# Kernel tuning notes

Measured on AMD Instinct MI355X. Metric: run time of the kernel, lower is better.

## Reference

```python
import jax, jax.numpy as jnp
import numpy as np

OUTPUT_SEQ_LEN = 64


def setup_inputs() -> dict:
    key = jax.random.key(0)
    ks = jax.random.split(key, 12)
    S, B, H, O = 256, 256, 512, 64  # src_len, batch, hidden, output vocab
    sos_token = jax.random.normal(ks[0], (1, B, O), dtype=jnp.float32)
    h = jax.random.normal(ks[1], (1, B, H), dtype=jnp.float32)
    encoder_outputs = jax.random.normal(ks[2], (S, B, H), dtype=jnp.float32)
    s = 0.05
    params = {
        'Wa': jax.random.normal(ks[3], (2 * H, H), dtype=jnp.float32) * s,  # attn linear
        'ba': jnp.zeros((H,), dtype=jnp.float32),
        'v': jax.random.normal(ks[4], (H,), dtype=jnp.float32) * s,          # scoring vector
        'W_ih': jax.random.normal(ks[5], (H, O + H), dtype=jnp.float32) * s,
        'b_ih': jnp.zeros((H,), dtype=jnp.float32),
        'W_hh': jax.random.normal(ks[6], (H, H), dtype=jnp.float32) * s,
        'b_hh': jnp.zeros((H,), dtype=jnp.float32),
        'Wo': jax.random.normal(ks[7], (O, H), dtype=jnp.float32) * s,       # output linear
        'bo': jnp.zeros((O,), dtype=jnp.float32),
    }
    return {'sos_token': sos_token, 'h': h, 'encoder_outputs': encoder_outputs, **params}


def reference(sos_token, h, encoder_outputs, Wa, ba, v, W_ih, b_ih, W_hh, b_hh, Wo, bo):
    # predict=True path of Decoder.forward: greedy argmax feedback each step.
    O = sos_token.shape[-1]
    h0 = h[0]                      # [B, H]
    x0 = sos_token[0]              # [B, O]

    def step(carry, _):
        h_t, x_t = carry           # [B,H], [B,O]
        # Bahdanau attention: score over source positions (softmax over dim 0)
        hid = jnp.broadcast_to(h_t[None], encoder_outputs.shape)          # [S,B,H]
        energy = jnp.tanh(jnp.concatenate([hid, encoder_outputs], axis=2) @ Wa + ba)  # [S,B,H]
        score = energy @ v                                                # [S,B]
        attn = jax.nn.softmax(score, axis=0)                              # [S,B]
        context = jnp.einsum('sb,sbh->bh', attn, encoder_outputs)         # [B,H]
        # single-layer vanilla RNN cell
        rnn_in = jnp.concatenate([x_t, context], axis=1)                  # [B,O+H]
        h_new = jnp.tanh(rnn_in @ W_ih.T + b_ih + h_t @ W_hh.T + b_hh)    # [B,H]
        out = h_new @ Wo.T + bo                                           # [B,O]
        # greedy feedback: one_hot(argmax(softmax(out))) == one_hot(argmax(out))
        x_next = jax.nn.one_hot(jnp.argmax(out, axis=1), O, dtype=out.dtype)
        return (h_new, x_next), out

    _, outs = jax.lax.scan(step, (h0, x0), None, length=OUTPUT_SEQ_LEN)   # [T,B,O]
    preds = outs[: OUTPUT_SEQ_LEN - 1]                                    # [T-1,B,O]
    preds = jnp.transpose(preds, (1, 2, 0))                               # [B,O,T-1]
    return preds
```

## Files before the change

kernel.cpp:

```cpp
#include <hip/hip_runtime.h>
#include <math.h>

#define SS 256
#define BB 256
#define HH 512
#define OO 64
#define NSTEP 63

__global__ __launch_bounds__(256) void k_ew_gemm(const float* __restrict__ A,
                                                 const float* __restrict__ Bm,
                                                 float* __restrict__ C)
{
    __shared__ float As[8][132];
    __shared__ float Bs[8][132];
    const int tid = threadIdx.x;
    const int bm = blockIdx.x * 128;
    const int bn = blockIdx.y * 128;
    const int tx = tid & 15;
    const int ty = tid >> 4;
    const int a_row = tid >> 1;
    const int a_k4 = (tid & 1) * 4;
    const int b_row = tid >> 5;
    const int b_n4 = (tid & 31) * 4;

    float acc[8][8];
#pragma unroll
    for (int i = 0; i < 8; i++)
#pragma unroll
        for (int j = 0; j < 8; j++) acc[i][j] = 0.f;

    for (int kt = 0; kt < 512; kt += 8) {
        float4 av = *(const float4*)(A + (size_t)(bm + a_row) * 512 + kt + a_k4);
        As[a_k4 + 0][a_row] = av.x;
        As[a_k4 + 1][a_row] = av.y;
        As[a_k4 + 2][a_row] = av.z;
        As[a_k4 + 3][a_row] = av.w;
        *(float4*)(&Bs[b_row][b_n4]) = *(const float4*)(Bm + (size_t)(kt + b_row) * 512 + bn + b_n4);
        __syncthreads();
#pragma unroll
        for (int kk = 0; kk < 8; kk++) {
            float av8[8], bv8[8];
            *(float4*)&av8[0] = *(const float4*)&As[kk][ty * 4];
            *(float4*)&av8[4] = *(const float4*)&As[kk][64 + ty * 4];
            *(float4*)&bv8[0] = *(const float4*)&Bs[kk][tx * 4];
            *(float4*)&bv8[4] = *(const float4*)&Bs[kk][64 + tx * 4];
#pragma unroll
            for (int i = 0; i < 8; i++)
#pragma unroll
                for (int j = 0; j < 8; j++) acc[i][j] += av8[i] * bv8[j];
        }
        __syncthreads();
    }
#pragma unroll
    for (int i = 0; i < 8; i++) {
        int m = bm + ((i < 4) ? (ty * 4 + i) : (64 + ty * 4 + i - 4));
        int mrow = (m & 255) * 256 + (m >> 8);
        float4 o0 = make_float4(acc[i][0], acc[i][1], acc[i][2], acc[i][3]);
        float4 o1 = make_float4(acc[i][4], acc[i][5], acc[i][6], acc[i][7]);
        *(float4*)(C + (size_t)mrow * 512 + bn + tx * 4) = o0;
        *(float4*)(C + (size_t)mrow * 512 + bn + 64 + tx * 4) = o1;
    }
}

__global__ __launch_bounds__(256) void k_qinit(const float* __restrict__ A,
                                               const float* __restrict__ Wa,
                                               float* __restrict__ qpre)
{
    __shared__ float As[32][33];
    __shared__ float Bs[32][33];
    const int tid = threadIdx.x;
    const int bn = blockIdx.x * 32;
    const int bm = blockIdx.y * 32;
    const int tx = tid & 15;
    const int ty = tid >> 4;
    const int l_row = tid >> 3;
    const int l_c4 = (tid & 7) * 4;

    float acc00 = 0.f, acc01 = 0.f, acc10 = 0.f, acc11 = 0.f;
    for (int kt = 0; kt < 512; kt += 32) {
#pragma unroll
        for (int i = 0; i < 4; i++)
            As[l_c4 + i][l_row] = A[(size_t)(bm + l_row) * 512 + kt + l_c4 + i];
#pragma unroll
        for (int i = 0; i < 4; i++)
            Bs[l_row][l_c4 + i] = Wa[(size_t)(kt + l_row) * 512 + bn + l_c4 + i];
        __syncthreads();
#pragma unroll
        for (int kk = 0; kk < 32; kk++) {
            float a0 = As[kk][ty * 2], a1 = As[kk][ty * 2 + 1];
            float b0 = Bs[kk][tx * 2], b1 = Bs[kk][tx * 2 + 1];
            acc00 += a0 * b0; acc01 += a0 * b1;
            acc10 += a1 * b0; acc11 += a1 * b1;
        }
        __syncthreads();
    }
    qpre[(size_t)(bm + ty * 2) * 512 + bn + tx * 2]     = acc00;
    qpre[(size_t)(bm + ty * 2) * 512 + bn + tx * 2 + 1] = acc01;
    qpre[(size_t)(bm + ty * 2 + 1) * 512 + bn + tx * 2]     = acc10;
    qpre[(size_t)(bm + ty * 2 + 1) * 512 + bn + tx * 2 + 1] = acc11;
}

__global__ __launch_bounds__(1024) void k_attn(const float* __restrict__ EW,
                                               const float* __restrict__ enc,
                                               const float* __restrict__ qpre,
                                               const float* __restrict__ ba,
                                               const float* __restrict__ vvec,
                                               float* __restrict__ ctx,
                                               float* __restrict__ hpre_out,
                                               float* __restrict__ ob)
{
    __shared__ float qs[512];
    __shared__ float vs[512];
    __shared__ float sc[256];
    __shared__ float red[16];
    __shared__ float ctxp[16][512];
    const int b = blockIdx.x;
    const int tid = threadIdx.x;

    if (tid < 576) {
        int idx = b * 576 + tid;
        if (idx < 131072) hpre_out[idx] = 0.f;
        else              ob[idx - 131072] = 0.f;
    }

    if (tid < 512) {
        qs[tid] = qpre[b * 512 + tid] + ba[tid];
        vs[tid] = vvec[tid];
    }
    __syncthreads();

    const int w = tid >> 6;
    const int l = tid & 63;

    float qv[8], vv[8];
    *(float4*)&qv[0] = *(const float4*)&qs[l * 8];
    *(float4*)&qv[4] = *(const float4*)&qs[l * 8 + 4];
    *(float4*)&vv[0] = *(const float4*)&vs[l * 8];
    *(float4*)&vv[4] = *(const float4*)&vs[l * 8 + 4];

    {
        const float4* pe = (const float4*)(EW + ((size_t)b * 256 + w * 16) * 512);
        for (int i = 0; i < 16; i += 2) {
            float4 e00 = pe[(size_t)i * 128 + 2 * l];
            float4 e01 = pe[(size_t)i * 128 + 2 * l + 1];
            float4 e10 = pe[(size_t)(i + 1) * 128 + 2 * l];
            float4 e11 = pe[(size_t)(i + 1) * 128 + 2 * l + 1];
            float a0, a1;
            a0  = vv[0] * tanhf(e00.x + qv[0]);
            a0 += vv[1] * tanhf(e00.y + qv[1]);
            a0 += vv[2] * tanhf(e00.z + qv[2]);
            a0 += vv[3] * tanhf(e00.w + qv[3]);
            a0 += vv[4] * tanhf(e01.x + qv[4]);
            a0 += vv[5] * tanhf(e01.y + qv[5]);
            a0 += vv[6] * tanhf(e01.z + qv[6]);
            a0 += vv[7] * tanhf(e01.w + qv[7]);
            a1  = vv[0] * tanhf(e10.x + qv[0]);
            a1 += vv[1] * tanhf(e10.y + qv[1]);
            a1 += vv[2] * tanhf(e10.z + qv[2]);
            a1 += vv[3] * tanhf(e10.w + qv[3]);
            a1 += vv[4] * tanhf(e11.x + qv[4]);
            a1 += vv[5] * tanhf(e11.y + qv[5]);
            a1 += vv[6] * tanhf(e11.z + qv[6]);
            a1 += vv[7] * tanhf(e11.w + qv[7]);
#pragma unroll
            for (int off = 32; off; off >>= 1) {
                a0 += __shfl_down(a0, off);
                a1 += __shfl_down(a1, off);
            }
            if (l == 0) {
                sc[w * 16 + i]     = a0;
                sc[w * 16 + i + 1] = a1;
            }
        }
    }
    __syncthreads();

    if (tid < 256) {
        float m = sc[tid];
#pragma unroll
        for (int off = 32; off; off >>= 1) m = fmaxf(m, __shfl_down(m, off));
        if ((tid & 63) == 0) red[tid >> 6] = m;
    }
    __syncthreads();
    if (tid < 256) {
        float mx = fmaxf(fmaxf(red[0], red[1]), fmaxf(red[2], red[3]));
        float e = expf(sc[tid] - mx);
        sc[tid] = e;
        float ssum = e;
#pragma unroll
        for (int off = 32; off; off >>= 1) ssum += __shfl_down(ssum, off);
        if ((tid & 63) == 0) red[8 + (tid >> 6)] = ssum;
    }
    __syncthreads();
    const float inv = 1.0f / (red[8] + red[9] + red[10] + red[11]);

    {
        float c[8];
#pragma unroll
        for (int j = 0; j < 8; j++) c[j] = 0.f;
        for (int i = 0; i < 16; i += 2) {
            int s0 = w * 16 + i;
            int s1 = s0 + 1;
            float w0 = sc[s0];
            float w1 = sc[s1];
            const float4* p0 = (const float4*)(enc + ((size_t)s0 * 256 + b) * 512);
            const float4* p1 = (const float4*)(enc + ((size_t)s1 * 256 + b) * 512);
            float4 e00 = p0[2 * l];
            float4 e01 = p0[2 * l + 1];
            float4 e10 = p1[2 * l];
            float4 e11 = p1[2 * l + 1];
            c[0] += w0 * e00.x; c[1] += w0 * e00.y;
            c[2] += w0 * e00.z; c[3] += w0 * e00.w;
            c[4] += w0 * e01.x; c[5] += w0 * e01.y;
            c[6] += w0 * e01.z; c[7] += w0 * e01.w;
            c[0] += w1 * e10.x; c[1] += w1 * e10.y;
            c[2] += w1 * e10.z; c[3] += w1 * e10.w;
            c[4] += w1 * e11.x; c[5] += w1 * e11.y;
            c[6] += w1 * e11.z; c[7] += w1 * e11.w;
        }
        float4 c0 = make_float4(c[0], c[1], c[2], c[3]);
        float4 c1 = make_float4(c[4], c[5], c[6], c[7]);
        *(float4*)&ctxp[w][l * 8]     = c0;
        *(float4*)&ctxp[w][l * 8 + 4] = c1;
    }
    __syncthreads();
    if (tid < 512) {
        float r = 0.f;
#pragma unroll
        for (int g = 0; g < 16; g++) r += ctxp[g][tid];
        ctx[b * 512 + tid] = r * inv;
    }
}

__global__ __launch_bounds__(256) void k_h(
    const float* __restrict__ xin, const float* __restrict__ ctx,
    const float* __restrict__ hpre_in, const float* __restrict__ h0,
    int t0,
    const float* __restrict__ W_ih, const float* __restrict__ W_hh,
    const float* __restrict__ b_ih, const float* __restrict__ b_hh,
    float* __restrict__ hpre_out, float* __restrict__ qpre)
{
    __shared__ float As[8][34];
    __shared__ float Bs[8][68];
    const int tid = threadIdx.x;
    const int bn = blockIdx.x * 64;
    const int bm = blockIdx.y * 32;
    const int k0 = blockIdx.z * 136;

    {
        int lin = ((blockIdx.z * 8 + blockIdx.y) * 8 + blockIdx.x) * 256 + tid;
        qpre[lin] = 0.f;
    }

    const int tx = tid & 15;
    const int ty = tid >> 4;
    const int sa_k = tid & 7;
    const int sa_m = tid >> 3;
    const int sb_n = tid >> 2;
    const int sb_k = (tid & 3) * 2;

    float acc[2][4];
#pragma unroll
    for (int i = 0; i < 2; i++)
#pragma unroll
        for (int j = 0; j < 4; j++) acc[i][j] = 0.f;

    for (int kt = 0; kt < 17; kt++) {
        const int kb = k0 + kt * 8;
        {
            int m = bm + sa_m;
            int k = kb + sa_k;
            float v;
            if (k < 64) v = xin[m * 64 + k];
            else if (k < 576) v = ctx[m * 512 + (k - 64)];
            else {
                int kh = k - 576;
                v = t0 ? h0[m * 512 + kh]
                       : tanhf(hpre_in[m * 512 + kh] + b_ih[kh] + b_hh[kh]);
            }
            As[sa_k][sa_m] = v;
        }
        {
            int n = bn + sb_n;
#pragma unroll
            for (int i = 0; i < 2; i++) {
                int k = kb + sb_k + i;
                float v = (k < 576) ? W_ih[(size_t)n * 576 + k]
                                    : W_hh[(size_t)n * 512 + (k - 576)];
                Bs[sb_k + i][sb_n] = v;
            }
        }
        __syncthreads();
#pragma unroll
        for (int kk = 0; kk < 8; kk++) {
            float a0 = As[kk][ty * 2], a1 = As[kk][ty * 2 + 1];
            float b0 = Bs[kk][tx * 4], b1 = Bs[kk][tx * 4 + 1];
            float b2 = Bs[kk][tx * 4 + 2], b3 = Bs[kk][tx * 4 + 3];
            acc[0][0] += a0 * b0; acc[0][1] += a0 * b1;
            acc[0][2] += a0 * b2; acc[0][3] += a0 * b3;
            acc[1][0] += a1 * b0; acc[1][1] += a1 * b1;
            acc[1][2] += a1 * b2; acc[1][3] += a1 * b3;
        }
        __syncthreads();
    }
#pragma unroll
    for (int i = 0; i < 2; i++) {
        int m = bm + ty * 2 + i;
#pragma unroll
        for (int j = 0; j < 4; j++) {
            atomicAdd(&hpre_out[(size_t)m * 512 + bn + tx * 4 + j], acc[i][j]);
        }
    }
}

__global__ __launch_bounds__(256) void k_outq(
    const float* __restrict__ hpre_cur,
    const float* __restrict__ b_ih, const float* __restrict__ b_hh,
    const float* __restrict__ Wo, const float* __restrict__ Wa,
    float* __restrict__ ob, float* __restrict__ qpre)
{
    __shared__ float As[8][34];
    __shared__ float Bs[8][68];
    const int tid = threadIdx.x;
    const int bn = blockIdx.x * 64;
    const int bm = blockIdx.y * 32;
    const int k0 = blockIdx.z * 128;
    const bool is_out = (bn < 64);

    const int tx = tid & 15;
    const int ty = tid >> 4;
    const int sa_k = tid & 7;
    const int sa_m = tid >> 3;
    const int sb_n = tid >> 2;
    const int sb_k = (tid & 3) * 2;
    const int qa_k = tid >> 5;
    const int qa_n = (tid & 31) * 2;

    float acc[2][4];
#pragma unroll
    for (int i = 0; i < 2; i++)
#pragma unroll
        for (int j = 0; j < 4; j++) acc[i][j] = 0.f;

    for (int kt = 0; kt < 16; kt++) {
        const int kb = k0 + kt * 8;
        {
            int m = bm + sa_m;
            int k = kb + sa_k;
            As[sa_k][sa_m] = tanhf(hpre_cur[(size_t)m * 512 + k] + b_ih[k] + b_hh[k]);
        }
        if (is_out) {
            int n = bn + sb_n;
#pragma unroll
            for (int i = 0; i < 2; i++) {
                int k = kb + sb_k + i;
                Bs[sb_k + i][sb_n] = Wo[(size_t)n * 512 + k];
            }
        } else {
            int k = kb + qa_k;
            int n = bn - 64 + qa_n;
#pragma unroll
            for (int i = 0; i < 2; i++)
                Bs[qa_k][qa_n + i] = Wa[(size_t)k * 512 + n + i];
        }
        __syncthreads();
#pragma unroll
        for (int kk = 0; kk < 8; kk++) {
            float a0 = As[kk][ty * 2], a1 = As[kk][ty * 2 + 1];
            float b0 = Bs[kk][tx * 4], b1 = Bs[kk][tx * 4 + 1];
            float b2 = Bs[kk][tx * 4 + 2], b3 = Bs[kk][tx * 4 + 3];
            acc[0][0] += a0 * b0; acc[0][1] += a0 * b1;
            acc[0][2] += a0 * b2; acc[0][3] += a0 * b3;
            acc[1][0] += a1 * b0; acc[1][1] += a1 * b1;
            acc[1][2] += a1 * b2; acc[1][3] += a1 * b3;
        }
        __syncthreads();
    }
#pragma unroll
    for (int i = 0; i < 2; i++) {
        int m = bm + ty * 2 + i;
#pragma unroll
        for (int j = 0; j < 4; j++) {
            int n = bn + tx * 4 + j;
            if (is_out) atomicAdd(&ob[m * 64 + n], acc[i][j]);
            else        atomicAdd(&qpre[(size_t)m * 512 + (n - 64)], acc[i][j]);
        }
    }
}

__global__ __launch_bounds__(256) void k_argmax(const float* __restrict__ ob,
                                                const float* __restrict__ bo,
                                                float* __restrict__ dout, int t,
                                                float* __restrict__ x)
{
    const int b = blockIdx.x * 4 + (threadIdx.x >> 6);
    const int l = threadIdx.x & 63;
    float v = ob[b * 64 + l] + bo[l];
    dout[(size_t)b * (OO * NSTEP) + l * NSTEP + t] = v;
    int bi = l;
    float bv = v;
#pragma unroll
    for (int off = 1; off < 64; off <<= 1) {
        float ov = __shfl_xor(bv, off);
        int oi = __shfl_xor(bi, off);
        if (ov > bv || (ov == bv && oi < bi)) { bv = ov; bi = oi; }
    }
    x[b * 64 + l] = (l == bi) ? 1.0f : 0.0f;
}

extern "C" void kernel_launch(void* const* d_in, const int* in_sizes, int n_in,
                              void* d_out, int out_size, void* d_ws, size_t ws_size,
                              hipStream_t stream)
{
    const float* sos  = (const float*)d_in[0];
    const float* h0   = (const float*)d_in[1];
    const float* enc  = (const float*)d_in[2];
    const float* Wa   = (const float*)d_in[3];
    const float* ba   = (const float*)d_in[4];
    const float* vvec = (const float*)d_in[5];
    const float* W_ih = (const float*)d_in[6];
    const float* b_ih = (const float*)d_in[7];
    const float* W_hh = (const float*)d_in[8];
    const float* b_hh = (const float*)d_in[9];
    const float* Wo   = (const float*)d_in[10];
    const float* bo   = (const float*)d_in[11];
    float* out = (float*)d_out;

    float* ws = (float*)d_ws;
    float* EW    = ws; ws += (size_t)SS * BB * HH;
    float* qpre  = ws; ws += BB * HH;
    float* ctx   = ws; ws += BB * HH;
    float* hpre0 = ws; ws += BB * HH;
    float* hpre1 = ws; ws += BB * HH;
    float* xb    = ws; ws += BB * OO;
    float* ob    = ws; ws += BB * OO;

    k_ew_gemm<<<dim3(512, 4), 256, 0, stream>>>(enc, Wa + 512 * 512, EW);
    k_qinit<<<dim3(16, 8), 256, 0, stream>>>(h0, Wa, qpre);

    for (int t = 0; t < NSTEP; t++) {
        float* hpre_out = (t & 1) ? hpre1 : hpre0;
        float* hpre_in  = (t & 1) ? hpre0 : hpre1;
        const float* xin = (t == 0) ? sos : xb;

        k_attn<<<256, 1024, 0, stream>>>(EW, enc, qpre, ba, vvec, ctx,
                                         hpre_out, ob);

        k_h<<<dim3(8, 8, 8), 256, 0, stream>>>(xin, ctx, hpre_in, h0, (t == 0) ? 1 : 0,
                                               W_ih, W_hh, b_ih, b_hh,
                                               hpre_out, qpre);

        k_outq<<<dim3(9, 8, 4), 256, 0, stream>>>(hpre_out, b_ih, b_hh,
                                                  Wo, Wa, ob, qpre);

        k_argmax<<<64, 256, 0, stream>>>(ob, bo, out, t, xb);
    }
}
```

Before: 7.324 ms.

## Fuse argmax into attention kernel and use nontemporal loads for EW stream

Moves the per-step argmax/output write into the start of the next step's attention kernel, dropping one launch per step, and adds a single trailing argmax launch for the last step. The ob zeroing moves into k_h. The EW store and EW loads become nontemporal, and the score and context loops are unrolled to four rows per iteration to raise memory-level parallelism. This risks extra register pressure in the 1024-thread attention kernel, and the nontemporal hints may not help if EW would otherwise stay resident in cache.

```diff
diff --git a/kernel.cpp b/kernel.cpp
--- a/kernel.cpp
+++ b/kernel.cpp
@@ -6,6 +6,15 @@
 #define HH 512
 #define OO 64
 #define NSTEP 63
+
+typedef float f32x4 __attribute__((ext_vector_type(4)));
+
+__device__ __forceinline__ f32x4 nt_load4(const float* p) {
+    return __builtin_nontemporal_load((const f32x4*)p);
+}
+__device__ __forceinline__ void nt_store4(float* p, f32x4 v) {
+    __builtin_nontemporal_store(v, (f32x4*)p);
+}
 
 __global__ __launch_bounds__(256) void k_ew_gemm(const float* __restrict__ A,
                                                  const float* __restrict__ Bm,
@@ -55,10 +64,10 @@
     for (int i = 0; i < 8; i++) {
         int m = bm + ((i < 4) ? (ty * 4 + i) : (64 + ty * 4 + i - 4));
         int mrow = (m & 255) * 256 + (m >> 8);
-        float4 o0 = make_float4(acc[i][0], acc[i][1], acc[i][2], acc[i][3]);
-        float4 o1 = make_float4(acc[i][4], acc[i][5], acc[i][6], acc[i][7]);
-        *(float4*)(C + (size_t)mrow * 512 + bn + tx * 4) = o0;
-        *(float4*)(C + (size_t)mrow * 512 + bn + 64 + tx * 4) = o1;
+        f32x4 o0 = { acc[i][0], acc[i][1], acc[i][2], acc[i][3] };
+        f32x4 o1 = { acc[i][4], acc[i][5], acc[i][6], acc[i][7] };
+        nt_store4(C + (size_t)mrow * 512 + bn + tx * 4, o0);
+        nt_store4(C + (size_t)mrow * 512 + bn + 64 + tx * 4, o1);
     }
 }
 
@@ -107,7 +116,11 @@
                                                const float* __restrict__ vvec,
                                                float* __restrict__ ctx,
                                                float* __restrict__ hpre_out,
-                                               float* __restrict__ ob)
+                                               const float* __restrict__ ob,
+                                               const float* __restrict__ bo,
+                                               float* __restrict__ dout,
+                                               float* __restrict__ xb,
+                                               int t)
 {
     __shared__ float qs[512];
     __shared__ float vs[512];
@@ -117,10 +130,24 @@
     const int b = blockIdx.x;
     const int tid = threadIdx.x;
 
+    if (t > 0 && tid < 64) {
+        const int l = tid;
+        float v = ob[b * 64 + l] + bo[l];
+        dout[(size_t)b * (OO * NSTEP) + l * NSTEP + (t - 1)] = v;
+        int bi = l;
+        float bv = v;
+#pragma unroll
+        for (int off = 1; off < 64; off <<= 1) {
+            float ov = __shfl_xor(bv, off);
+            int oi = __shfl_xor(bi, off);
+            if (ov > bv || (ov == bv && oi < bi)) { bv = ov; bi = oi; }
+        }
+        xb[b * 64 + l] = (l == bi) ? 1.0f : 0.0f;
+    }
+
     if (tid < 576) {
         int idx = b * 576 + tid;
         if (idx < 131072) hpre_out[idx] = 0.f;
-        else              ob[idx - 131072] = 0.f;
     }
 
     if (tid < 512) {
@@ -139,37 +166,42 @@
     *(float4*)&vv[4] = *(const float4*)&vs[l * 8 + 4];
 
     {
-        const float4* pe = (const float4*)(EW + ((size_t)b * 256 + w * 16) * 512);
-        for (int i = 0; i < 16; i += 2) {
-            float4 e00 = pe[(size_t)i * 128 + 2 * l];
-            float4 e01 = pe[(size_t)i * 128 + 2 * l + 1];
-            float4 e10 = pe[(size_t)(i + 1) * 128 + 2 * l];
-            float4 e11 = pe[(size_t)(i + 1) * 128 + 2 * l + 1];
-            float a0, a1;
-            a0  = vv[0] * tanhf(e00.x + qv[0]);
-            a0 += vv[1] * tanhf(e00.y + qv[1]);
-            a0 += vv[2] * tanhf(e00.z + qv[2]);
-            a0 += vv[3] * tanhf(e00.w + qv[3]);
-            a0 += vv[4] * tanhf(e01.x + qv[4]);
-            a0 += vv[5] * tanhf(e01.y + qv[5]);
-            a0 += vv[6] * tanhf(e01.z + qv[6]);
-            a0 += vv[7] * tanhf(e01.w + qv[7]);
-            a1  = vv[0] * tanhf(e10.x + qv[0]);
-            a1 += vv[1] * tanhf(e10.y + qv[1]);
-            a1 += vv[2] * tanhf(e10.z + qv[2]);
-            a1 += vv[3] * tanhf(e10.w + qv[3]);
-            a1 += vv[4] * tanhf(e11.x + qv[4]);
-            a1 += vv[5] * tanhf(e11.y + qv[5]);
-            a1 += vv[6] * tanhf(e11.z + qv[6]);
-            a1 += vv[7] * tanhf(e11.w + qv[7]);
+        const float* base = EW + ((size_t)b * 256 + w * 16) * 512 + l * 8;
+        for (int i = 0; i < 16; i += 4) {
+            f32x4 e[8];
+#pragma unroll
+            for (int r = 0; r < 4; r++) {
+                const float* rp = base + (size_t)(i + r) * 512;
+                e[2 * r]     = nt_load4(rp);
+                e[2 * r + 1] = nt_load4(rp + 4);
+            }
+            float a[4];
+#pragma unroll
+            for (int r = 0; r < 4; r++) {
+                f32x4 e0 = e[2 * r], e1 = e[2 * r + 1];
+                float s;
+                s  = vv[0] * tanhf(e0.x + qv[0]);
+                s += vv[1] * tanhf(e0.y + qv[1]);
+                s += vv[2] * tanhf(e0.z + qv[2]);
+                s += vv[3] * tanhf(e0.w + qv[3]);
+                s += vv[4] * tanhf(e1.x + qv[4]);
+                s += vv[5] * tanhf(e1.y + qv[5]);
+                s += vv[6] * tanhf(e1.z + qv[6]);
+                s += vv[7] * tanhf(e1.w + qv[7]);
+                a[r] = s;
+            }
 #pragma unroll
             for (int off = 32; off; off >>= 1) {
-                a0 += __shfl_down(a0, off);
-                a1 += __shfl_down(a1, off);
+                a[0] += __shfl_down(a[0], off);
+                a[1] += __shfl_down(a[1], off);
+                a[2] += __shfl_down(a[2], off);
+                a[3] += __shfl_down(a[3], off);
             }
             if (l == 0) {
-                sc[w * 16 + i]     = a0;
-                sc[w * 16 + i + 1] = a1;
+                sc[w * 16 + i]     = a[0];
+                sc[w * 16 + i + 1] = a[1];
+                sc[w * 16 + i + 2] = a[2];
+                sc[w * 16 + i + 3] = a[3];
             }
         }
     }
@@ -198,25 +230,20 @@
         float c[8];
 #pragma unroll
         for (int j = 0; j < 8; j++) c[j] = 0.f;
-        for (int i = 0; i < 16; i += 2) {
-            int s0 = w * 16 + i;
-            int s1 = s0 + 1;
-            float w0 = sc[s0];
-            float w1 = sc[s1];
-            const float4* p0 = (const float4*)(enc + ((size_t)s0 * 256 + b) * 512);
-            const float4* p1 = (const float4*)(enc + ((size_t)s1 * 256 + b) * 512);
-            float4 e00 = p0[2 * l];
-            float4 e01 = p0[2 * l + 1];
-            float4 e10 = p1[2 * l];
-            float4 e11 = p1[2 * l + 1];
-            c[0] += w0 * e00.x; c[1] += w0 * e00.y;
-            c[2] += w0 * e00.z; c[3] += w0 * e00.w;
-            c[4] += w0 * e01.x; c[5] += w0 * e01.y;
-            c[6] += w0 * e01.z; c[7] += w0 * e01.w;
-            c[0] += w1 * e10.x; c[1] += w1 * e10.y;
-            c[2] += w1 * e10.z; c[3] += w1 * e10.w;
-            c[4] += w1 * e11.x; c[5] += w1 * e11.y;
-            c[6] += w1 * e11.z; c[7] += w1 * e11.w;
+        const float* basee = enc + (size_t)b * 512 + l * 8;
+        for (int i = 0; i < 16; i += 4) {
+#pragma unroll
+            for (int r = 0; r < 4; r++) {
+                int s = w * 16 + i + r;
+                float wt = sc[s];
+                const float4* p = (const float4*)(basee + (size_t)s * (256 * 512));
+                float4 e0 = p[0];
+                float4 e1 = p[1];
+                c[0] += wt * e0.x; c[1] += wt * e0.y;
+                c[2] += wt * e0.z; c[3] += wt * e0.w;
+                c[4] += wt * e1.x; c[5] += wt * e1.y;
+                c[6] += wt * e1.z; c[7] += wt * e1.w;
+            }
         }
         float4 c0 = make_float4(c[0], c[1], c[2], c[3]);
         float4 c1 = make_float4(c[4], c[5], c[6], c[7]);
@@ -238,7 +265,8 @@
     int t0,
     const float* __restrict__ W_ih, const float* __restrict__ W_hh,
     const float* __restrict__ b_ih, const float* __restrict__ b_hh,
-    float* __restrict__ hpre_out, float* __restrict__ qpre)
+    float* __restrict__ hpre_out, float* __restrict__ qpre,
+    float* __restrict__ ob)
 {
     __shared__ float As[8][34];
     __shared__ float Bs[8][68];
@@ -250,6 +278,10 @@
     {
         int lin = ((blockIdx.z * 8 + blockIdx.y) * 8 + blockIdx.x) * 256 + tid;
         qpre[lin] = 0.f;
+    }
+    if (blockIdx.z == 7) {
+        int lin = (blockIdx.y * 8 + blockIdx.x) * 256 + tid;
+        ob[lin] = 0.f;
     }
 
     const int tx = tid & 15;
@@ -444,15 +476,15 @@
         const float* xin = (t == 0) ? sos : xb;
 
         k_attn<<<256, 1024, 0, stream>>>(EW, enc, qpre, ba, vvec, ctx,
-                                         hpre_out, ob);
+                                         hpre_out, ob, bo, out, xb, t);
 
         k_h<<<dim3(8, 8, 8), 256, 0, stream>>>(xin, ctx, hpre_in, h0, (t == 0) ? 1 : 0,
                                                W_ih, W_hh, b_ih, b_hh,
-                                               hpre_out, qpre);
+                                               hpre_out, qpre, ob);
 
         k_outq<<<dim3(9, 8, 4), 256, 0, stream>>>(hpre_out, b_ih, b_hh,
                                                   Wo, Wa, ob, qpre);
-
-        k_argmax<<<64, 256, 0, stream>>>(ob, bo, out, t, xb);
-    }
-}
+    }
+
+    k_argmax<<<64, 256, 0, stream>>>(ob, bo, out, NSTEP - 1, xb);
+}
```

New measurement: 7.503 ms. 2.4% more time.

## Fuse per-step decoder kernels into one persistent cooperative kernel with grid sync

Applied to the files above, without the earlier changes.

Replaces the four per-timestep launches (attention, hidden GEMM, output/query GEMM, argmax) with a single cooperative kernel of 256 blocks that loops over all steps, separated by grid-wide syncs. The split-K atomic accumulation is replaced by full-K tiles owned by one block each, so no zeroing passes or atomics are needed, and tanh is applied once when h is written. This removes about 250 launch gaps and the atomic traffic. In exchange, each GEMM phase runs on only 256 (or 144) blocks with one output element per thread and less parallelism, and there are three grid barriers per step.

```diff
diff --git a/kernel.cpp b/kernel.cpp
--- a/kernel.cpp
+++ b/kernel.cpp
@@ -1,4 +1,5 @@
 #include <hip/hip_runtime.h>
+#include <hip/hip_cooperative_groups.h>
 #include <math.h>
 
 #define SS 256
@@ -6,6 +7,8 @@
 #define HH 512
 #define OO 64
 #define NSTEP 63
+
+namespace cg = cooperative_groups;
 
 __global__ __launch_bounds__(256) void k_ew_gemm(const float* __restrict__ A,
                                                  const float* __restrict__ Bm,
@@ -100,312 +103,260 @@
     qpre[(size_t)(bm + ty * 2 + 1) * 512 + bn + tx * 2 + 1] = acc11;
 }
 
-__global__ __launch_bounds__(1024) void k_attn(const float* __restrict__ EW,
-                                               const float* __restrict__ enc,
-                                               const float* __restrict__ qpre,
-                                               const float* __restrict__ ba,
-                                               const float* __restrict__ vvec,
-                                               float* __restrict__ ctx,
-                                               float* __restrict__ hpre_out,
-                                               float* __restrict__ ob)
-{
-    __shared__ float qs[512];
-    __shared__ float vs[512];
-    __shared__ float sc[256];
-    __shared__ float red[16];
-    __shared__ float ctxp[16][512];
-    const int b = blockIdx.x;
-    const int tid = threadIdx.x;
-
-    if (tid < 576) {
-        int idx = b * 576 + tid;
-        if (idx < 131072) hpre_out[idx] = 0.f;
-        else              ob[idx - 131072] = 0.f;
-    }
-
-    if (tid < 512) {
-        qs[tid] = qpre[b * 512 + tid] + ba[tid];
-        vs[tid] = vvec[tid];
-    }
-    __syncthreads();
-
-    const int w = tid >> 6;
-    const int l = tid & 63;
-
-    float qv[8], vv[8];
-    *(float4*)&qv[0] = *(const float4*)&qs[l * 8];
-    *(float4*)&qv[4] = *(const float4*)&qs[l * 8 + 4];
-    *(float4*)&vv[0] = *(const float4*)&vs[l * 8];
-    *(float4*)&vv[4] = *(const float4*)&vs[l * 8 + 4];
-
-    {
-        const float4* pe = (const float4*)(EW + ((size_t)b * 256 + w * 16) * 512);
-        for (int i = 0; i < 16; i += 2) {
-            float4 e00 = pe[(size_t)i * 128 + 2 * l];
-            float4 e01 = pe[(size_t)i * 128 + 2 * l + 1];
-            float4 e10 = pe[(size_t)(i + 1) * 128 + 2 * l];
-            float4 e11 = pe[(size_t)(i + 1) * 128 + 2 * l + 1];
-            float a0, a1;
-            a0  = vv[0] * tanhf(e00.x + qv[0]);
-            a0 += vv[1] * tanhf(e00.y + qv[1]);
-            a0 += vv[2] * tanhf(e00.z + qv[2]);
-            a0 += vv[3] * tanhf(e00.w + qv[3]);
-            a0 += vv[4] * tanhf(e01.x + qv[4]);
-            a0 += vv[5] * tanhf(e01.y + qv[5]);
-            a0 += vv[6] * tanhf(e01.z + qv[6]);
-            a0 += vv[7] * tanhf(e01.w + qv[7]);
-            a1  = vv[0] * tanhf(e10.x + qv[0]);
-            a1 += vv[1] * tanhf(e10.y + qv[1]);
-            a1 += vv[2] * tanhf(e10.z + qv[2]);
-            a1 += vv[3] * tanhf(e10.w + qv[3]);
-            a1 += vv[4] * tanhf(e11.x + qv[4]);
-            a1 += vv[5] * tanhf(e11.y + qv[5]);
-            a1 += vv[6] * tanhf(e11.z + qv[6]);
-            a1 += vv[7] * tanhf(e11.w + qv[7]);
-#pragma unroll
-            for (int off = 32; off; off >>= 1) {
-                a0 += __shfl_down(a0, off);
-                a1 += __shfl_down(a1, off);
-            }
-            if (l == 0) {
-                sc[w * 16 + i]     = a0;
-                sc[w * 16 + i + 1] = a1;
-            }
-        }
-    }
-    __syncthreads();
-
-    if (tid < 256) {
-        float m = sc[tid];
-#pragma unroll
-        for (int off = 32; off; off >>= 1) m = fmaxf(m, __shfl_down(m, off));
-        if ((tid & 63) == 0) red[tid >> 6] = m;
-    }
-    __syncthreads();
-    if (tid < 256) {
-        float mx = fmaxf(fmaxf(red[0], red[1]), fmaxf(red[2], red[3]));
-        float e = expf(sc[tid] - mx);
-        sc[tid] = e;
-        float ssum = e;
-#pragma unroll
-        for (int off = 32; off; off >>= 1) ssum += __shfl_down(ssum, off);
-        if ((tid & 63) == 0) red[8 + (tid >> 6)] = ssum;
-    }
-    __syncthreads();
-    const float inv = 1.0f / (red[8] + red[9] + red[10] + red[11]);
-
-    {
-        float c[8];
-#pragma unroll
-        for (int j = 0; j < 8; j++) c[j] = 0.f;
-        for (int i = 0; i < 16; i += 2) {
-            int s0 = w * 16 + i;
-            int s1 = s0 + 1;
-            float w0 = sc[s0];
-            float w1 = sc[s1];
-            const float4* p0 = (const float4*)(enc + ((size_t)s0 * 256 + b) * 512);
-            const float4* p1 = (const float4*)(enc + ((size_t)s1 * 256 + b) * 512);
-            float4 e00 = p0[2 * l];
-            float4 e01 = p0[2 * l + 1];
-            float4 e10 = p1[2 * l];
-            float4 e11 = p1[2 * l + 1];
-            c[0] += w0 * e00.x; c[1] += w0 * e00.y;
-            c[2] += w0 * e00.z; c[3] += w0 * e00.w;
-            c[4] += w0 * e01.x; c[5] += w0 * e01.y;
-            c[6] += w0 * e01.z; c[7] += w0 * e01.w;
-            c[0] += w1 * e10.x; c[1] += w1 * e10.y;
-            c[2] += w1 * e10.z; c[3] += w1 * e10.w;
-            c[4] += w1 * e11.x; c[5] += w1 * e11.y;
-            c[6] += w1 * e11.z; c[7] += w1 * e11.w;
-        }
-        float4 c0 = make_float4(c[0], c[1], c[2], c[3]);
-        float4 c1 = make_float4(c[4], c[5], c[6], c[7]);
-        *(float4*)&ctxp[w][l * 8]     = c0;
-        *(float4*)&ctxp[w][l * 8 + 4] = c1;
-    }
-    __syncthreads();
-    if (tid < 512) {
-        float r = 0.f;
-#pragma unroll
-        for (int g = 0; g < 16; g++) r += ctxp[g][tid];
-        ctx[b * 512 + tid] = r * inv;
-    }
-}
-
-__global__ __launch_bounds__(256) void k_h(
-    const float* __restrict__ xin, const float* __restrict__ ctx,
-    const float* __restrict__ hpre_in, const float* __restrict__ h0,
-    int t0,
+__global__ __launch_bounds__(1024) void k_loop(
+    const float* __restrict__ EW, const float* __restrict__ enc,
+    float* __restrict__ qpre, const float* __restrict__ ba,
+    const float* __restrict__ vvec, float* __restrict__ ctx,
+    const float* __restrict__ h0, const float* __restrict__ sos,
+    float* __restrict__ xb, float* __restrict__ hb0, float* __restrict__ hb1,
     const float* __restrict__ W_ih, const float* __restrict__ W_hh,
     const float* __restrict__ b_ih, const float* __restrict__ b_hh,
-    float* __restrict__ hpre_out, float* __restrict__ qpre)
+    const float* __restrict__ Wo, const float* __restrict__ Wa,
+    const float* __restrict__ bo, float* __restrict__ ob,
+    float* __restrict__ dout)
 {
-    __shared__ float As[8][34];
-    __shared__ float Bs[8][68];
+    cg::grid_group grid = cg::this_grid();
+    __shared__ float smem[9488];
+    const int blk = blockIdx.x;
     const int tid = threadIdx.x;
-    const int bn = blockIdx.x * 64;
-    const int bm = blockIdx.y * 32;
-    const int k0 = blockIdx.z * 136;
-
-    {
-        int lin = ((blockIdx.z * 8 + blockIdx.y) * 8 + blockIdx.x) * 256 + tid;
-        qpre[lin] = 0.f;
+
+    for (int t = 0; t < NSTEP; t++) {
+        const float* hprev = (t == 0) ? h0 : ((t & 1) ? hb0 : hb1);
+        float* hcur = (t & 1) ? hb1 : hb0;
+        const float* xin = (t == 0) ? sos : xb;
+
+        {
+            const int b = blk;
+            float* qs   = smem;
+            float* vs   = smem + 512;
+            float* sc   = smem + 1024;
+            float* red  = smem + 1280;
+            float* ctxp = smem + 1296;
+
+            if (t > 0 && tid < 64) {
+                const int l = tid;
+                float v = ob[b * 64 + l] + bo[l];
+                dout[(size_t)b * (OO * NSTEP) + l * NSTEP + (t - 1)] = v;
+                int bi = l;
+                float bv = v;
+#pragma unroll
+                for (int off = 1; off < 64; off <<= 1) {
+                    float ov = __shfl_xor(bv, off);
+                    int oi = __shfl_xor(bi, off);
+                    if (ov > bv || (ov == bv && oi < bi)) { bv = ov; bi = oi; }
+                }
+                xb[b * 64 + l] = (l == bi) ? 1.0f : 0.0f;
+            }
+
+            if (tid < 512) {
+                qs[tid] = qpre[b * 512 + tid] + ba[tid];
+                vs[tid] = vvec[tid];
+            }
+            __syncthreads();
+
+            const int w = tid >> 6;
+            const int l = tid & 63;
+
+            float qv[8], vv[8];
+            *(float4*)&qv[0] = *(const float4*)&qs[l * 8];
+            *(float4*)&qv[4] = *(const float4*)&qs[l * 8 + 4];
+            *(float4*)&vv[0] = *(const float4*)&vs[l * 8];
+            *(float4*)&vv[4] = *(const float4*)&vs[l * 8 + 4];
+
+            {
+                const float4* pe = (const float4*)(EW + ((size_t)b * 256 + w * 16) * 512);
+                for (int i = 0; i < 16; i += 2) {
+                    float4 e00 = pe[(size_t)i * 128 + 2 * l];
+                    float4 e01 = pe[(size_t)i * 128 + 2 * l + 1];
+                    float4 e10 = pe[(size_t)(i + 1) * 128 + 2 * l];
+                    float4 e11 = pe[(size_t)(i + 1) * 128 + 2 * l + 1];
+                    float a0, a1;
+                    a0  = vv[0] * tanhf(e00.x + qv[0]);
+                    a0 += vv[1] * tanhf(e00.y + qv[1]);
+                    a0 += vv[2] * tanhf(e00.z + qv[2]);
+                    a0 += vv[3] * tanhf(e00.w + qv[3]);
+                    a0 += vv[4] * tanhf(e01.x + qv[4]);
+                    a0 += vv[5] * tanhf(e01.y + qv[5]);
+                    a0 += vv[6] * tanhf(e01.z + qv[6]);
+                    a0 += vv[7] * tanhf(e01.w + qv[7]);
+                    a1  = vv[0] * tanhf(e10.x + qv[0]);
+                    a1 += vv[1] * tanhf(e10.y + qv[1]);
+                    a1 += vv[2] * tanhf(e10.z + qv[2]);
+                    a1 += vv[3] * tanhf(e10.w + qv[3]);
+                    a1 += vv[4] * tanhf(e11.x + qv[4]);
+                    a1 += vv[5] * tanhf(e11.y + qv[5]);
+                    a1 += vv[6] * tanhf(e11.z + qv[6]);
+                    a1 += vv[7] * tanhf(e11.w + qv[7]);
+#pragma unroll
+                    for (int off = 32; off; off >>= 1) {
+                        a0 += __shfl_down(a0, off);
+                        a1 += __shfl_down(a1, off);
+                    }
+                    if (l == 0) {
+                        sc[w * 16 + i]     = a0;
+                        sc[w * 16 + i + 1] = a1;
+                    }
+                }
+            }
+            __syncthreads();
+
+            if (tid < 256) {
+                float m = sc[tid];
+#pragma unroll
+                for (int off = 32; off; off >>= 1) m = fmaxf(m, __shfl_down(m, off));
+                if ((tid & 63) == 0) red[tid >> 6] = m;
+            }
+            __syncthreads();
+            if (tid < 256) {
+                float mx = fmaxf(fmaxf(red[0], red[1]), fmaxf(red[2], red[3]));
+                float e = expf(sc[tid] - mx);
+                sc[tid] = e;
+                float ssum = e;
+#pragma unroll
+                for (int off = 32; off; off >>= 1) ssum += __shfl_down(ssum, off);
+                if ((tid & 63) == 0) red[8 + (tid >> 6)] = ssum;
+            }
+            __syncthreads();
+            const float inv = 1.0f / (red[8] + red[9] + red[10] + red[11]);
+
+            {
+                float c[8];
+#pragma unroll
+                for (int j = 0; j < 8; j++) c[j] = 0.f;
+                for (int i = 0; i < 16; i += 2) {
+                    int s0 = w * 16 + i;
+                    int s1 = s0 + 1;
+                    float w0 = sc[s0];
+                    float w1 = sc[s1];
+                    const float4* p0 = (const float4*)(enc + ((size_t)s0 * 256 + b) * 512);
+                    const float4* p1 = (const float4*)(enc + ((size_t)s1 * 256 + b) * 512);
+                    float4 e00 = p0[2 * l];
+                    float4 e01 = p0[2 * l + 1];
+                    float4 e10 = p1[2 * l];
+                    float4 e11 = p1[2 * l + 1];
+                    c[0] += w0 * e00.x; c[1] += w0 * e00.y;
+                    c[2] += w0 * e00.z; c[3] += w0 * e00.w;
+                    c[4] += w0 * e01.x; c[5] += w0 * e01.y;
+                    c[6] += w0 * e01.z; c[7] += w0 * e01.w;
+                    c[0] += w1 * e10.x; c[1] += w1 * e10.y;
+                    c[2] += w1 * e10.z; c[3] += w1 * e10.w;
+                    c[4] += w1 * e11.x; c[5] += w1 * e11.y;
+                    c[6] += w1 * e11.z; c[7] += w1 * e11.w;
+                }
+                float4 c0 = make_float4(c[0], c[1], c[2], c[3]);
+                float4 c1 = make_float4(c[4], c[5], c[6], c[7]);
+                *(float4*)&ctxp[w * 512 + l * 8]     = c0;
+                *(float4*)&ctxp[w * 512 + l * 8 + 4] = c1;
+            }
+            __syncthreads();
+            if (tid < 512) {
+                float r = 0.f;
+#pragma unroll
+                for (int g = 0; g < 16; g++) r += ctxp[g * 512 + tid];
+                ctx[b * 512 + tid] = r * inv;
+            }
+        }
+        __threadfence();
+        grid.sync();
+
+        {
+            const int mt = blk >> 4, nt = blk & 15;
+            const int m0 = mt * 16, n0 = nt * 32;
+            float* As  = smem;
+            float* Bs  = smem + 1088;
+            float* red = smem + 3200;
+            const int am = tid >> 6, ak = tid & 63;
+            const int o = tid & 511, kh = tid >> 9;
+            const int om = o >> 5, on = o & 31;
+            float acc = 0.f;
+
+            for (int c = 0; c < 17; c++) {
+                const int k0 = c * 64;
+                __syncthreads();
+                {
+                    int k = k0 + ak, m = m0 + am;
+                    float v;
+                    if (k < 64) v = xin[m * 64 + k];
+                    else if (k < 576) v = ctx[m * 512 + (k - 64)];
+                    else v = hprev[m * 512 + (k - 576)];
+                    As[ak * 17 + am] = v;
+                }
+#pragma unroll
+                for (int it = 0; it < 2; it++) {
+                    int j = tid + it * 1024;
+                    int n = j >> 6, kk = j & 63;
+                    int k = k0 + kk, ng = n0 + n;
+                    float v = (k < 576) ? W_ih[(size_t)ng * 576 + k]
+                                        : W_hh[(size_t)ng * 512 + (k - 576)];
+                    Bs[kk * 33 + n] = v;
+                }
+                __syncthreads();
+#pragma unroll
+                for (int kk2 = 0; kk2 < 32; kk2++) {
+                    int kk = kh * 32 + kk2;
+                    acc += As[kk * 17 + om] * Bs[kk * 33 + on];
+                }
+            }
+            __syncthreads();
+            if (kh == 1) red[o] = acc;
+            __syncthreads();
+            if (kh == 0) {
+                int ng = n0 + on, mg = m0 + om;
+                float s = acc + red[o];
+                hcur[mg * 512 + ng] = tanhf(s + b_ih[ng] + b_hh[ng]);
+            }
+        }
+        __threadfence();
+        grid.sync();
+
+        {
+            if (blk < 144) {
+                const int mt = blk / 9, nt = blk % 9;
+                const int m0 = mt * 16, n0 = nt * 64;
+                float* As = smem;
+                float* Bs = smem + 1088;
+                const int am = tid >> 6, ak = tid & 63;
+                const int om = tid >> 6, on = tid & 63;
+                float acc = 0.f;
+
+                for (int c = 0; c < 8; c++) {
+                    const int k0 = c * 64;
+                    __syncthreads();
+                    As[ak * 17 + am] = hcur[(m0 + am) * 512 + k0 + ak];
+                    if (nt == 0) {
+#pragma unroll
+                        for (int it = 0; it < 4; it++) {
+                            int j = tid + it * 1024;
+                            int n = j >> 6, kk = j & 63;
+                            Bs[kk * 65 + n] = Wo[(size_t)(n0 + n) * 512 + k0 + kk];
+                        }
+                    } else {
+#pragma unroll
+                        for (int it = 0; it < 4; it++) {
+                            int j = tid + it * 1024;
+                            int kk = j >> 6, n = j & 63;
+                            Bs[kk * 65 + n] = Wa[(size_t)(k0 + kk) * 512 + (n0 - 64) + n];
+                        }
+                    }
+                    __syncthreads();
+#pragma unroll
+                    for (int kk = 0; kk < 64; kk++)
+                        acc += As[kk * 17 + om] * Bs[kk * 65 + on];
+                }
+                int mg = m0 + om;
+                if (nt == 0) ob[mg * 64 + on] = acc;
+                else         qpre[(size_t)mg * 512 + (n0 - 64) + on] = acc;
+            }
+        }
+        __threadfence();
+        grid.sync();
     }
 
-    const int tx = tid & 15;
-    const int ty = tid >> 4;
-    const int sa_k = tid & 7;
-    const int sa_m = tid >> 3;
-    const int sb_n = tid >> 2;
-    const int sb_k = (tid & 3) * 2;
-
-    float acc[2][4];
-#pragma unroll
-    for (int i = 0; i < 2; i++)
-#pragma unroll
-        for (int j = 0; j < 4; j++) acc[i][j] = 0.f;
-
-    for (int kt = 0; kt < 17; kt++) {
-        const int kb = k0 + kt * 8;
-        {
-            int m = bm + sa_m;
-            int k = kb + sa_k;
-            float v;
-            if (k < 64) v = xin[m * 64 + k];
-            else if (k < 576) v = ctx[m * 512 + (k - 64)];
-            else {
-                int kh = k - 576;
-                v = t0 ? h0[m * 512 + kh]
-                       : tanhf(hpre_in[m * 512 + kh] + b_ih[kh] + b_hh[kh]);
-            }
-            As[sa_k][sa_m] = v;
-        }
-        {
-            int n = bn + sb_n;
-#pragma unroll
-            for (int i = 0; i < 2; i++) {
-                int k = kb + sb_k + i;
-                float v = (k < 576) ? W_ih[(size_t)n * 576 + k]
-                                    : W_hh[(size_t)n * 512 + (k - 576)];
-                Bs[sb_k + i][sb_n] = v;
-            }
-        }
-        __syncthreads();
-#pragma unroll
-        for (int kk = 0; kk < 8; kk++) {
-            float a0 = As[kk][ty * 2], a1 = As[kk][ty * 2 + 1];
-            float b0 = Bs[kk][tx * 4], b1 = Bs[kk][tx * 4 + 1];
-            float b2 = Bs[kk][tx * 4 + 2], b3 = Bs[kk][tx * 4 + 3];
-            acc[0][0] += a0 * b0; acc[0][1] += a0 * b1;
-            acc[0][2] += a0 * b2; acc[0][3] += a0 * b3;
-            acc[1][0] += a1 * b0; acc[1][1] += a1 * b1;
-            acc[1][2] += a1 * b2; acc[1][3] += a1 * b3;
-        }
-        __syncthreads();
+    if (tid < 64) {
+        const int b = blk, l = tid;
+        float v = ob[b * 64 + l] + bo[l];
+        dout[(size_t)b * (OO * NSTEP) + l * NSTEP + (NSTEP - 1)] = v;
     }
-#pragma unroll
-    for (int i = 0; i < 2; i++) {
-        int m = bm + ty * 2 + i;
-#pragma unroll
-        for (int j = 0; j < 4; j++) {
-            atomicAdd(&hpre_out[(size_t)m * 512 + bn + tx * 4 + j], acc[i][j]);
-        }
-    }
-}
-
-__global__ __launch_bounds__(256) void k_outq(
-    const float* __restrict__ hpre_cur,
-    const float* __restrict__ b_ih, const float* __restrict__ b_hh,
-    const float* __restrict__ Wo, const float* __restrict__ Wa,
-    float* __restrict__ ob, float* __restrict__ qpre)
-{
-    __shared__ float As[8][34];
-    __shared__ float Bs[8][68];
-    const int tid = threadIdx.x;
-    const int bn = blockIdx.x * 64;
-    const int bm = blockIdx.y * 32;
-    const int k0 = blockIdx.z * 128;
-    const bool is_out = (bn < 64);
-
-    const int tx = tid & 15;
-    const int ty = tid >> 4;
-    const int sa_k = tid & 7;
-    const int sa_m = tid >> 3;
-    const int sb_n = tid >> 2;
-    const int sb_k = (tid & 3) * 2;
-    const int qa_k = tid >> 5;
-    const int qa_n = (tid & 31) * 2;
-
-    float acc[2][4];
-#pragma unroll
-    for (int i = 0; i < 2; i++)
-#pragma unroll
-        for (int j = 0; j < 4; j++) acc[i][j] = 0.f;
-
-    for (int kt = 0; kt < 16; kt++) {
-        const int kb = k0 + kt * 8;
-        {
-            int m = bm + sa_m;
-            int k = kb + sa_k;
-            As[sa_k][sa_m] = tanhf(hpre_cur[(size_t)m * 512 + k] + b_ih[k] + b_hh[k]);
-        }
-        if (is_out) {
-            int n = bn + sb_n;
-#pragma unroll
-            for (int i = 0; i < 2; i++) {
-                int k = kb + sb_k + i;
-                Bs[sb_k + i][sb_n] = Wo[(size_t)n * 512 + k];
-            }
-        } else {
-            int k = kb + qa_k;
-            int n = bn - 64 + qa_n;
-#pragma unroll
-            for (int i = 0; i < 2; i++)
-                Bs[qa_k][qa_n + i] = Wa[(size_t)k * 512 + n + i];
-        }
-        __syncthreads();
-#pragma unroll
-        for (int kk = 0; kk < 8; kk++) {
-            float a0 = As[kk][ty * 2], a1 = As[kk][ty * 2 + 1];
-            float b0 = Bs[kk][tx * 4], b1 = Bs[kk][tx * 4 + 1];
-            float b2 = Bs[kk][tx * 4 + 2], b3 = Bs[kk][tx * 4 + 3];
-            acc[0][0] += a0 * b0; acc[0][1] += a0 * b1;
-            acc[0][2] += a0 * b2; acc[0][3] += a0 * b3;
-            acc[1][0] += a1 * b0; acc[1][1] += a1 * b1;
-            acc[1][2] += a1 * b2; acc[1][3] += a1 * b3;
-        }
-        __syncthreads();
-    }
-#pragma unroll
-    for (int i = 0; i < 2; i++) {
-        int m = bm + ty * 2 + i;
-#pragma unroll
-        for (int j = 0; j < 4; j++) {
-            int n = bn + tx * 4 + j;
-            if (is_out) atomicAdd(&ob[m * 64 + n], acc[i][j]);
-            else        atomicAdd(&qpre[(size_t)m * 512 + (n - 64)], acc[i][j]);
-        }
-    }
-}
-
-__global__ __launch_bounds__(256) void k_argmax(const float* __restrict__ ob,
-                                                const float* __restrict__ bo,
-                                                float* __restrict__ dout, int t,
-                                                float* __restrict__ x)
-{
-    const int b = blockIdx.x * 4 + (threadIdx.x >> 6);
-    const int l = threadIdx.x & 63;
-    float v = ob[b * 64 + l] + bo[l];
-    dout[(size_t)b * (OO * NSTEP) + l * NSTEP + t] = v;
-    int bi = l;
-    float bv = v;
-#pragma unroll
-    for (int off = 1; off < 64; off <<= 1) {
-        float ov = __shfl_xor(bv, off);
-        int oi = __shfl_xor(bi, off);
-        if (ov > bv || (ov == bv && oi < bi)) { bv = ov; bi = oi; }
-    }
-    x[b * 64 + l] = (l == bi) ? 1.0f : 0.0f;
 }
 
 extern "C" void kernel_launch(void* const* d_in, const int* in_sizes, int n_in,
@@ -427,32 +378,23 @@
     float* out = (float*)d_out;
 
     float* ws = (float*)d_ws;
-    float* EW    = ws; ws += (size_t)SS * BB * HH;
-    float* qpre  = ws; ws += BB * HH;
-    float* ctx   = ws; ws += BB * HH;
-    float* hpre0 = ws; ws += BB * HH;
-    float* hpre1 = ws; ws += BB * HH;
-    float* xb    = ws; ws += BB * OO;
-    float* ob    = ws; ws += BB * OO;
+    float* EW   = ws; ws += (size_t)SS * BB * HH;
+    float* qpre = ws; ws += BB * HH;
+    float* ctx  = ws; ws += BB * HH;
+    float* hb0  = ws; ws += BB * HH;
+    float* hb1  = ws; ws += BB * HH;
+    float* xb   = ws; ws += BB * OO;
+    float* ob   = ws; ws += BB * OO;
 
     k_ew_gemm<<<dim3(512, 4), 256, 0, stream>>>(enc, Wa + 512 * 512, EW);
     k_qinit<<<dim3(16, 8), 256, 0, stream>>>(h0, Wa, qpre);
 
-    for (int t = 0; t < NSTEP; t++) {
-        float* hpre_out = (t & 1) ? hpre1 : hpre0;
-        float* hpre_in  = (t & 1) ? hpre0 : hpre1;
-        const float* xin = (t == 0) ? sos : xb;
-
-        k_attn<<<256, 1024, 0, stream>>>(EW, enc, qpre, ba, vvec, ctx,
-                                         hpre_out, ob);
-
-        k_h<<<dim3(8, 8, 8), 256, 0, stream>>>(xin, ctx, hpre_in, h0, (t == 0) ? 1 : 0,
-                                               W_ih, W_hh, b_ih, b_hh,
-                                               hpre_out, qpre);
-
-        k_outq<<<dim3(9, 8, 4), 256, 0, stream>>>(hpre_out, b_ih, b_hh,
-                                                  Wo, Wa, ob, qpre);
-
-        k_argmax<<<64, 256, 0, stream>>>(ob, bo, out, t, xb);
-    }
+    void* args[] = {
+        (void*)&EW, (void*)&enc, (void*)&qpre, (void*)&ba, (void*)&vvec,
+        (void*)&ctx, (void*)&h0, (void*)&sos, (void*)&xb, (void*)&hb0,
+        (void*)&hb1, (void*)&W_ih, (void*)&W_hh, (void*)&b_ih, (void*)&b_hh,
+        (void*)&Wo, (void*)&Wa, (void*)&bo, (void*)&ob, (void*)&out
+    };
+    hipLaunchCooperativeKernel((void*)k_loop, dim3(256), dim3(1024),
+                               args, 0, stream);
 }
```

Result: slower. 29.05 ms (+296.6%).
